# Performance work log

Measured on AMD Instinct MI355X. Metric: run time of the kernel, lower is better.

Reference implementation:

```python
import jax, jax.numpy as jnp
import numpy as np

EPS = 1e-5

def _make_mask(rng, outdim, indim, expand_size, k=3):
    # Mirrors ExpanderConv2d mask construction (indim <= outdim branch when equal)
    m = np.zeros((outdim, indim), dtype=np.float32)
    if indim > outdim:
        for i in range(outdim):
            idx = rng.permutation(indim)[:expand_size]
            m[i, idx] = 1.0
    else:
        for i in range(indim):
            idx = rng.permutation(outdim)[:expand_size]
            m[idx, i] = 1.0
    return jnp.asarray(np.broadcast_to(m[:, :, None, None], (outdim, indim, k, k)).copy())

def _bn(x, gamma, beta, mean, var):
    # eval-mode BatchNorm2d over channel axis (NCHW)
    inv = gamma / jnp.sqrt(var + EPS)
    return x * inv[None, :, None, None] + (beta - mean * inv)[None, :, None, None]

def _conv3x3(x, w, stride=1):
    return jax.lax.conv_general_dilated(
        x, w, window_strides=(stride, stride), padding=((1, 1), (1, 1)),
        dimension_numbers=('NCHW', 'OIHW', 'NCHW'))

def setup_inputs() -> dict:
    key = jax.random.key(0)
    ks = jax.random.split(key, 4)
    C = 256
    x = jax.random.normal(ks[0], (64, C, 32, 32), dtype=jnp.float32)
    fan_out = C * 9
    std = float(np.sqrt(2.0 / fan_out))  # kaiming_normal_, mode='fan_out'
    w1 = jax.random.normal(ks[1], (C, C, 3, 3), dtype=jnp.float32) * std
    w2 = jax.random.normal(ks[2], (C, C, 3, 3), dtype=jnp.float32) * std
    rng = np.random.default_rng(0)
    mask1 = _make_mask(rng, C, C, C // 8)
    mask2 = _make_mask(rng, C, C, C // 8)
    g = jax.random.uniform(ks[3], (4 * C,), minval=0.5, maxval=1.5, dtype=jnp.float32)
    return {
        'x': x,
        'bn1_gamma': g[:C], 'bn1_beta': jnp.zeros((C,), jnp.float32),
        'bn1_mean': jnp.zeros((C,), jnp.float32), 'bn1_var': jnp.ones((C,), jnp.float32),
        'w1': w1, 'mask1': mask1,
        'bn2_gamma': g[C:2 * C], 'bn2_beta': jnp.zeros((C,), jnp.float32),
        'bn2_mean': jnp.zeros((C,), jnp.float32), 'bn2_var': jnp.ones((C,), jnp.float32),
        'w2': w2, 'mask2': mask2,
    }

def reference(x, bn1_gamma, bn1_beta, bn1_mean, bn1_var, w1, mask1,
              bn2_gamma, bn2_beta, bn2_mean, bn2_var, w2, mask2):
    out = jax.nn.relu(_bn(x, bn1_gamma, bn1_beta, bn1_mean, bn1_var))
    out = _conv3x3(out, w1 * mask1)          # masked expander conv, dropout(p=0)=identity
    out = jax.nn.relu(_bn(out, bn2_gamma, bn2_beta, bn2_mean, bn2_var))
    out = _conv3x3(out, w2 * mask2, stride=1)
    return out + x                            # identity shortcut (stride=1, in==out)
```

## Files before the change

### kernel.cpp

```cpp
#include <hip/hip_runtime.h>
#include <hip/hip_bf16.h>
#include <stdint.h>

typedef __bf16 bf16_t;
typedef __bf16 bf16x8 __attribute__((ext_vector_type(8)));
typedef __bf16 bf16x4 __attribute__((ext_vector_type(4)));
typedef float  f32x4  __attribute__((ext_vector_type(4)));

#define AS_GLOBAL __attribute__((address_space(1)))
#define AS_LDS    __attribute__((address_space(3)))
#define VMW(N) asm volatile("s_waitcnt vmcnt(" #N ")" ::: "memory")

static constexpr int CCH   = 256;
static constexpr int HP    = 34;
static constexpr int PLANE = HP * HP;

__global__ void prep_params_k(const float* g1, const float* b1, const float* m1, const float* v1,
                              const float* g2, const float* b2, const float* m2, const float* v2,
                              float* prm) {
  int i = threadIdx.x;
  float i1 = g1[i] * rsqrtf(v1[i] + 1e-5f);
  prm[i]       = i1;
  prm[256 + i] = b1[i] - m1[i] * i1;
  float i2 = g2[i] * rsqrtf(v2[i] + 1e-5f);
  prm[512 + i] = i2;
  prm[768 + i] = b2[i] - m2[i] * i2;
}

__global__ __launch_bounds__(256) void prep_weights_k(const float* __restrict__ w,
                                                      const float* __restrict__ msk,
                                                      bf16_t* __restrict__ out) {
  int idx = blockIdx.x * 256 + threadIdx.x;
  const float* wp = w + (long)idx * 9;
  const float* mp = msk + (long)idx * 9;
#pragma unroll
  for (int khw = 0; khw < 9; ++khw)
    out[khw * 65536 + idx] = (bf16_t)(wp[khw] * mp[khw]);
}

__global__ __launch_bounds__(256) void zero_borders_k(bf16_t* __restrict__ t0p,
                                                      bf16_t* __restrict__ t1p) {
  const int bid = blockIdx.x;
  bf16_t* base = ((bid & 1) ? t1p : t0p) + (long)(bid >> 1) * PLANE * CCH;
  for (int i = threadIdx.x; i < 132 * 32; i += 256) {
    int pix = i >> 5, c16 = i & 31;
    int r, col;
    if (pix < 34)       { r = 0;           col = pix; }
    else if (pix < 68)  { r = 33;          col = pix - 34; }
    else if (pix < 100) { r = pix - 68 + 1; col = 0; }
    else                { r = pix - 100 + 1; col = 33; }
    *(f32x4*)&base[(r * HP + col) * CCH + c16 * 8] = f32x4{0.f, 0.f, 0.f, 0.f};
  }
}

__global__ __launch_bounds__(256) void prep_input_k(const float* __restrict__ x,
                                                    const float* __restrict__ prm,
                                                    bf16_t* __restrict__ t0p) {
  __shared__ __align__(16) bf16_t tile[64 * 256];
  const int tid = threadIdx.x;
  const int bid = blockIdx.x;
  const int n   = bid >> 4;
  const int p0  = (bid & 15) << 6;
  const int px    = tid & 63;
  const int cbase = tid >> 6;
  for (int r = 0; r < 64; ++r) {
    int ci = r * 4 + cbase;
    float v = x[((n * 256 + ci) << 10) + p0 + px];
    float y = fmaxf(v * prm[ci] + prm[256 + ci], 0.f);
    int byte = px * 512 + ((ci * 2) ^ ((px & 7) << 4));
    *(bf16_t*)((char*)tile + byte) = (bf16_t)y;
  }
  __syncthreads();
  for (int j = 0; j < 8; ++j) {
    int off  = j * 256 + tid;
    int pix  = off >> 5;
    int c16  = off & 31;
    int byte = pix * 512 + ((c16 * 16) ^ ((pix & 7) << 4));
    bf16x8 v = *(const bf16x8*)((char*)tile + byte);
    int p = p0 + pix;
    long gp = ((long)n * PLANE + ((p >> 5) + 1) * HP + (p & 31) + 1) * CCH + c16 * 8;
    *(bf16x8*)(t0p + gp) = v;
  }
}

template <int EPI>
__global__ __launch_bounds__(256, 2) void conv3x3_k(const bf16_t* __restrict__ inp,
                                                    const bf16_t* __restrict__ wts,
                                                    const float* __restrict__ prm,
                                                    const float* __restrict__ resid,
                                                    bf16_t* __restrict__ out_cl,
                                                    float* __restrict__ out_f) {
  __shared__ __align__(128) bf16_t As[5][4096];
  __shared__ __align__(128) bf16_t Bs[2][8192];

  const int tid  = threadIdx.x;
  const int lane = tid & 63;
  const int wid  = tid >> 6;
  const int wm   = wid >> 1;
  const int wn   = wid & 1;

  const int bid = blockIdx.x;
  const int w   = ((bid & 7) << 7) + (bid >> 3);
  const int co0 = (w & 1) << 7;
  const int pt  = w >> 1;
  const int n   = pt >> 3;
  const int hb  = (pt & 7) << 2;

  const int swz8 = (((lane & 3) ^ ((lane >> 2) & 3) ^ (lane >> 4)) << 3);
  const int l15  = lane & 15;
  const int k4   = lane >> 4;

  f32x4 acc[4][4];
#pragma unroll
  for (int i = 0; i < 4; ++i)
#pragma unroll
    for (int j = 0; j < 4; ++j) acc[i][j] = f32x4{0.f, 0.f, 0.f, 0.f};

  auto stageA = [&](int abuf, int c, int t) {
    const int ci0 = c << 5;
#pragma unroll
    for (int j = 0; j < 2; ++j) {
      const int ch  = wid * 2 + j;
      const int row = ch * 16 + (lane >> 2);
      const bf16_t* ga = wts + ((t * CCH + co0 + row) * CCH + ci0 + swz8);
      __builtin_amdgcn_global_load_lds((const AS_GLOBAL void*)ga,
                                       (AS_LDS void*)(&As[abuf][ch * 512]), 16, 0, 0);
    }
  };

  auto stageB = [&](int bbuf, int c) {
    const int ci0 = c << 5;
#pragma unroll
    for (int j = 0; j < 4; ++j) {
      const int ibase = wid * 4 + j;
      int s = (ibase << 6) + lane;
      if (s > 815) s = 815;
      const int r     = s / 136;
      const int rem   = s - r * 136;
      const int cc    = rem >> 2;
      const int k     = ((rem & 3) - (cc >> 1)) & 3;
      const bf16_t* gb = inp + ((n * PLANE + (hb + r) * HP + cc) * CCH + ci0 + (k << 3));
      __builtin_amdgcn_global_load_lds((const AS_GLOBAL void*)gb,
                                       (AS_LDS void*)(&Bs[bbuf][ibase * 512]), 16, 0, 0);
    }
  };

  auto compute = [&](int abuf, int bbuf, int kh, int kw) {
    bf16x8 av[4], bv[4];
#pragma unroll
    for (int mi = 0; mi < 4; ++mi)
      av[mi] = *(const bf16x8*)&As[abuf][((wm * 64 + mi * 16 + l15) << 5) + swz8];
#pragma unroll
    for (int ni = 0; ni < 4; ++ni) {
      const int p    = (wn << 6) + (ni << 4) + l15;
      const int cc   = (p & 31) + kw;
      const int slot = ((p >> 5) + kh) * 136 + (cc << 2) + ((k4 + (cc >> 1)) & 3);
      bv[ni] = *(const bf16x8*)&Bs[bbuf][slot << 3];
    }
#pragma unroll
    for (int mi = 0; mi < 4; ++mi)
#pragma unroll
      for (int ni = 0; ni < 4; ++ni)
        acc[mi][ni] = __builtin_amdgcn_mfma_f32_16x16x32_bf16(av[mi], bv[ni], acc[mi][ni], 0, 0, 0);
  };

  stageB(0, 0);
  stageA(0, 0, 0); stageA(1, 0, 1); stageA(2, 0, 2); stageA(3, 0, 3);

  int ab = 0;
  for (int c = 0; c < 7; ++c) {
#pragma unroll
    for (int t = 0; t < 9; ++t) {
      if (t >= 1 && t <= 3) { VMW(10); } else { VMW(6); }
      __builtin_amdgcn_s_barrier();
      if (t == 0) stageB((c + 1) & 1, c + 1);
      int aw = ab + 4; if (aw >= 5) aw -= 5;
      if (t < 5) stageA(aw, c, t + 4);
      else       stageA(aw, c + 1, t - 5);
      compute(ab, c & 1, t / 3, t % 3);
      ++ab; if (ab == 5) ab = 0;
    }
  }
#pragma unroll
  for (int t = 0; t < 9; ++t) {
    if      (t == 6) { VMW(4); }
    else if (t == 7) { VMW(2); }
    else if (t == 8) { VMW(0); }
    else             { VMW(6); }
    __builtin_amdgcn_s_barrier();
    if (t < 5) { int aw = ab + 4; if (aw >= 5) aw -= 5; stageA(aw, 7, t + 4); }
    compute(ab, 1, t / 3, t % 3);
    ++ab; if (ab == 5) ab = 0;
  }

  if (EPI == 0) {
#pragma unroll
    for (int mi = 0; mi < 4; ++mi) {
      const int co_b = co0 + wm * 64 + mi * 16 + ((lane >> 4) << 2);
      const float s0 = prm[co_b], s1 = prm[co_b + 1], s2 = prm[co_b + 2], s3 = prm[co_b + 3];
      const float t0 = prm[256 + co_b], t1 = prm[256 + co_b + 1],
                  t2 = prm[256 + co_b + 2], t3 = prm[256 + co_b + 3];
#pragma unroll
      for (int ni = 0; ni < 4; ++ni) {
        f32x4 v = acc[mi][ni];
        const int p  = (wn << 6) + (ni << 4) + l15;
        const int pr = p >> 5, pc = p & 31;
        bf16x4 pk;
        pk[0] = (bf16_t)fmaxf(v[0] * s0 + t0, 0.f);
        pk[1] = (bf16_t)fmaxf(v[1] * s1 + t1, 0.f);
        pk[2] = (bf16_t)fmaxf(v[2] * s2 + t2, 0.f);
        pk[3] = (bf16_t)fmaxf(v[3] * s3 + t3, 0.f);
        *(bf16x4*)&out_cl[(n * PLANE + (hb + pr + 1) * HP + pc + 1) * CCH + co_b] = pk;
      }
    }
  } else {
#pragma unroll
    for (int mi = 0; mi < 4; ++mi) {
      const int co_b = co0 + wm * 64 + mi * 16 + ((lane >> 4) << 2);
#pragma unroll
      for (int ni = 0; ni < 4; ++ni) {
        f32x4 v = acc[mi][ni];
        const int p  = (wn << 6) + (ni << 4) + l15;
        const int gp = ((n * CCH + co_b) << 10) + (hb << 5) + p;
        out_f[gp]        = v[0] + resid[gp];
        out_f[gp + 1024] = v[1] + resid[gp + 1024];
        out_f[gp + 2048] = v[2] + resid[gp + 2048];
        out_f[gp + 3072] = v[3] + resid[gp + 3072];
      }
    }
  }
}

extern "C" void kernel_launch(void* const* d_in, const int* in_sizes, int n_in,
                              void* d_out, int out_size, void* d_ws, size_t ws_size,
                              hipStream_t stream) {
  const float* x  = (const float*)d_in[0];
  const float* g1 = (const float*)d_in[1];
  const float* b1 = (const float*)d_in[2];
  const float* m1 = (const float*)d_in[3];
  const float* v1 = (const float*)d_in[4];
  const float* w1 = (const float*)d_in[5];
  const float* k1 = (const float*)d_in[6];
  const float* g2 = (const float*)d_in[7];
  const float* b2 = (const float*)d_in[8];
  const float* m2 = (const float*)d_in[9];
  const float* v2 = (const float*)d_in[10];
  const float* w2 = (const float*)d_in[11];
  const float* k2 = (const float*)d_in[12];

  char* ws = (char*)d_ws;
  const size_t T0P_B = (size_t)64 * PLANE * CCH * 2;
  bf16_t* t0p = (bf16_t*)ws;
  bf16_t* t1p = (bf16_t*)(ws + T0P_B);
  bf16_t* mw1 = (bf16_t*)(ws + 2 * T0P_B);
  bf16_t* mw2 = (bf16_t*)(ws + 2 * T0P_B + 1179648);
  float*  prm = (float*)(ws + 2 * T0P_B + 2 * 1179648);

  prep_params_k<<<1, 256, 0, stream>>>(g1, b1, m1, v1, g2, b2, m2, v2, prm);
  zero_borders_k<<<128, 256, 0, stream>>>(t0p, t1p);
  prep_weights_k<<<256, 256, 0, stream>>>(w1, k1, mw1);
  prep_weights_k<<<256, 256, 0, stream>>>(w2, k2, mw2);
  prep_input_k<<<1024, 256, 0, stream>>>(x, prm, t0p);

  conv3x3_k<0><<<1024, 256, 0, stream>>>(t0p, mw1, prm + 512, nullptr, t1p, nullptr);
  conv3x3_k<1><<<1024, 256, 0, stream>>>(t1p, mw2, nullptr, x, nullptr, (float*)d_out);
}
```

Before: 203.3 us.

## Double-buffer LDS fragment reads so next tap's loads overlap current MFMAs

Each tap's A/B fragments are now read from LDS into one of two register sets during the previous tap's iteration, and the MFMAs run on the other set. The whole K loop is fully unrolled with macros, and the vmcnt waits are retuned. The MFMA block is wrapped in setprio and a sched_barrier. The aim is to hide LDS read latency behind the matrix core work. The cost is higher register pressure and larger code, and the prefetch timing relative to the barriers has to stay correct for the buffer rotation.

```diff
diff --git a/kernel.cpp b/kernel.cpp
--- a/kernel.cpp
+++ b/kernel.cpp
@@ -116,6 +116,8 @@
 #pragma unroll
     for (int j = 0; j < 4; ++j) acc[i][j] = f32x4{0.f, 0.f, 0.f, 0.f};
 
+  bf16x8 avA[4], bvA[4], avB[4], bvB[4];
+
   auto stageA = [&](int abuf, int c, int t) {
     const int ci0 = c << 5;
 #pragma unroll
@@ -145,53 +147,74 @@
     }
   };
 
-  auto compute = [&](int abuf, int bbuf, int kh, int kw) {
-    bf16x8 av[4], bv[4];
-#pragma unroll
-    for (int mi = 0; mi < 4; ++mi)
-      av[mi] = *(const bf16x8*)&As[abuf][((wm * 64 + mi * 16 + l15) << 5) + swz8];
-#pragma unroll
-    for (int ni = 0; ni < 4; ++ni) {
-      const int p    = (wn << 6) + (ni << 4) + l15;
-      const int cc   = (p & 31) + kw;
-      const int slot = ((p >> 5) + kh) * 136 + (cc << 2) + ((k4 + (cc >> 1)) & 3);
-      bv[ni] = *(const bf16x8*)&Bs[bbuf][slot << 3];
-    }
-#pragma unroll
-    for (int mi = 0; mi < 4; ++mi)
-#pragma unroll
-      for (int ni = 0; ni < 4; ++ni)
-        acc[mi][ni] = __builtin_amdgcn_mfma_f32_16x16x32_bf16(av[mi], bv[ni], acc[mi][ni], 0, 0, 0);
-  };
+#define PREF(AV, BV, ABUF, BB, KH, KW) do {                                        \
+    _Pragma("unroll") for (int mi = 0; mi < 4; ++mi)                               \
+      AV[mi] = *(const bf16x8*)&As[ABUF][((wm * 64 + mi * 16 + l15) << 5) + swz8]; \
+    _Pragma("unroll") for (int ni = 0; ni < 4; ++ni) {                             \
+      const int p_    = (wn << 6) + (ni << 4) + l15;                               \
+      const int cc_   = (p_ & 31) + (KW);                                          \
+      const int slot_ = ((p_ >> 5) + (KH)) * 136 + (cc_ << 2) + ((k4 + (cc_ >> 1)) & 3); \
+      BV[ni] = *(const bf16x8*)&Bs[BB][slot_ << 3];                                \
+    }                                                                              \
+  } while (0)
+
+#define MFMA16(AV, BV) do {                                                        \
+    _Pragma("unroll") for (int mi = 0; mi < 4; ++mi)                               \
+    _Pragma("unroll") for (int ni = 0; ni < 4; ++ni)                               \
+      acc[mi][ni] = __builtin_amdgcn_mfma_f32_16x16x32_bf16(AV[mi], BV[ni], acc[mi][ni], 0, 0, 0); \
+  } while (0)
+
+#define PH(t, PAR, c, LAST) do {                                                   \
+    if ((LAST) && (t) >= 6) { if ((t) == 6) { VMW(2); } else { VMW(0); } }         \
+    else if (!(LAST) && ((t) == 1 || (t) == 2)) { VMW(8); }                        \
+    else { VMW(4); }                                                               \
+    __builtin_amdgcn_s_barrier();                                                  \
+    if (!(LAST) && (t) == 0) stageB(((c) + 1) & 1, (c) + 1);                       \
+    {                                                                              \
+      int aw = ab + 4; if (aw >= 5) aw -= 5;                                       \
+      if (!(LAST)) { if ((t) < 5) stageA(aw, (c), (t) + 4);                        \
+                     else         stageA(aw, (c) + 1, (t) - 5); }                  \
+      else if ((t) < 5) stageA(aw, 7, (t) + 4);                                    \
+    }                                                                              \
+    if (!((LAST) && (t) == 8)) {                                                   \
+      int ab1 = ab + 1; if (ab1 >= 5) ab1 -= 5;                                    \
+      const int bb1 = ((t) < 8 ? (c) & 1 : ((c) + 1) & 1);                         \
+      constexpr int T1 = ((t) + 1) % 9;                                            \
+      if (((PAR) + (t)) & 1) { PREF(avA, bvA, ab1, bb1, T1 / 3, T1 % 3); }         \
+      else                   { PREF(avB, bvB, ab1, bb1, T1 / 3, T1 % 3); }         \
+      asm volatile("s_waitcnt lgkmcnt(8)" ::: "memory");                           \
+    } else {                                                                       \
+      asm volatile("s_waitcnt lgkmcnt(0)" ::: "memory");                           \
+    }                                                                              \
+    __builtin_amdgcn_sched_barrier(0);                                             \
+    __builtin_amdgcn_s_setprio(1);                                                 \
+    if (((PAR) + (t)) & 1) { MFMA16(avB, bvB); } else { MFMA16(avA, bvA); }        \
+    __builtin_amdgcn_s_setprio(0);                                                 \
+    ++ab; if (ab == 5) ab = 0;                                                     \
+  } while (0)
+
+#define CHUNK(PAR, c) do {                                                         \
+    PH(0, PAR, c, 0); PH(1, PAR, c, 0); PH(2, PAR, c, 0);                          \
+    PH(3, PAR, c, 0); PH(4, PAR, c, 0); PH(5, PAR, c, 0);                          \
+    PH(6, PAR, c, 0); PH(7, PAR, c, 0); PH(8, PAR, c, 0);                          \
+  } while (0)
 
   stageB(0, 0);
   stageA(0, 0, 0); stageA(1, 0, 1); stageA(2, 0, 2); stageA(3, 0, 3);
+  VMW(6);
+  __builtin_amdgcn_s_barrier();
+  PREF(avA, bvA, 0, 0, 0, 0);
 
   int ab = 0;
-  for (int c = 0; c < 7; ++c) {
-#pragma unroll
-    for (int t = 0; t < 9; ++t) {
-      if (t >= 1 && t <= 3) { VMW(10); } else { VMW(6); }
-      __builtin_amdgcn_s_barrier();
-      if (t == 0) stageB((c + 1) & 1, c + 1);
-      int aw = ab + 4; if (aw >= 5) aw -= 5;
-      if (t < 5) stageA(aw, c, t + 4);
-      else       stageA(aw, c + 1, t - 5);
-      compute(ab, c & 1, t / 3, t % 3);
-      ++ab; if (ab == 5) ab = 0;
-    }
-  }
-#pragma unroll
-  for (int t = 0; t < 9; ++t) {
-    if      (t == 6) { VMW(4); }
-    else if (t == 7) { VMW(2); }
-    else if (t == 8) { VMW(0); }
-    else             { VMW(6); }
-    __builtin_amdgcn_s_barrier();
-    if (t < 5) { int aw = ab + 4; if (aw >= 5) aw -= 5; stageA(aw, 7, t + 4); }
-    compute(ab, 1, t / 3, t % 3);
-    ++ab; if (ab == 5) ab = 0;
-  }
+  CHUNK(0, 0); CHUNK(1, 1); CHUNK(0, 2); CHUNK(1, 3);
+  CHUNK(0, 4); CHUNK(1, 5); CHUNK(0, 6);
+  PH(0, 1, 7, 1); PH(1, 1, 7, 1); PH(2, 1, 7, 1); PH(3, 1, 7, 1); PH(4, 1, 7, 1);
+  PH(5, 1, 7, 1); PH(6, 1, 7, 1); PH(7, 1, 7, 1); PH(8, 1, 7, 1);
+
+#undef PH
+#undef CHUNK
+#undef PREF
+#undef MFMA16
 
   if (EPI == 0) {
 #pragma unroll
```

Measured after the change: 192.9 us. 1.05x faster.

## Shrink A-tile pipeline to double buffer, raise occupancy to 3 blocks, add setprio

Applied to the files above, without the earlier changes.

Cuts the weight (A) staging ring from five LDS buffers to two and raises launch bounds to allow three blocks per CU. The aim is to hide latency through extra waves instead of deep per-block prefetching. Waits are tightened to vmcnt(0)/vmcnt(4), so each block overlaps loads with compute less. MFMA sections are wrapped in s_setprio to favour the compute waves, and the outer chunk loop is no longer unrolled to save code size and registers.

```diff
diff --git a/kernel.cpp b/kernel.cpp
--- a/kernel.cpp
+++ b/kernel.cpp
@@ -84,13 +84,13 @@
 }
 
 template <int EPI>
-__global__ __launch_bounds__(256, 2) void conv3x3_k(const bf16_t* __restrict__ inp,
+__global__ __launch_bounds__(256, 3) void conv3x3_k(const bf16_t* __restrict__ inp,
                                                     const bf16_t* __restrict__ wts,
                                                     const float* __restrict__ prm,
                                                     const float* __restrict__ resid,
                                                     bf16_t* __restrict__ out_cl,
                                                     float* __restrict__ out_f) {
-  __shared__ __align__(128) bf16_t As[5][4096];
+  __shared__ __align__(128) bf16_t As[2][4096];
   __shared__ __align__(128) bf16_t Bs[2][8192];
 
   const int tid  = threadIdx.x;
@@ -145,53 +145,52 @@
     }
   };
 
-  auto compute = [&](int abuf, int bbuf, int kh, int kw) {
+  auto compute = [&](int ab, int bb, int kh, int kw) {
     bf16x8 av[4], bv[4];
 #pragma unroll
     for (int mi = 0; mi < 4; ++mi)
-      av[mi] = *(const bf16x8*)&As[abuf][((wm * 64 + mi * 16 + l15) << 5) + swz8];
+      av[mi] = *(const bf16x8*)&As[ab][((wm * 64 + mi * 16 + l15) << 5) + swz8];
 #pragma unroll
     for (int ni = 0; ni < 4; ++ni) {
       const int p    = (wn << 6) + (ni << 4) + l15;
       const int cc   = (p & 31) + kw;
       const int slot = ((p >> 5) + kh) * 136 + (cc << 2) + ((k4 + (cc >> 1)) & 3);
-      bv[ni] = *(const bf16x8*)&Bs[bbuf][slot << 3];
-    }
+      bv[ni] = *(const bf16x8*)&Bs[bb][slot << 3];
+    }
+    __builtin_amdgcn_s_setprio(1);
 #pragma unroll
     for (int mi = 0; mi < 4; ++mi)
 #pragma unroll
       for (int ni = 0; ni < 4; ++ni)
         acc[mi][ni] = __builtin_amdgcn_mfma_f32_16x16x32_bf16(av[mi], bv[ni], acc[mi][ni], 0, 0, 0);
+    __builtin_amdgcn_s_setprio(0);
   };
 
+#define PH(t, LASTC) do {                                                          \
+    if ((t) == 1 && !(LASTC)) { VMW(4); } else { VMW(0); }                         \
+    __builtin_amdgcn_s_barrier();                                                  \
+    {                                                                              \
+      const int pn = c * 9 + (t) + 1;                                              \
+      if (pn < 72) stageA(pn & 1, pn / 9, pn % 9);                                 \
+      if ((t) == 0 && !(LASTC)) stageB((c + 1) & 1, c + 1);                        \
+    }                                                                              \
+    compute((c * 9 + (t)) & 1, c & 1, (t) / 3, (t) % 3);                           \
+  } while (0)
+
   stageB(0, 0);
-  stageA(0, 0, 0); stageA(1, 0, 1); stageA(2, 0, 2); stageA(3, 0, 3);
-
-  int ab = 0;
+  stageA(0, 0, 0);
+
+#pragma unroll 1
   for (int c = 0; c < 7; ++c) {
-#pragma unroll
-    for (int t = 0; t < 9; ++t) {
-      if (t >= 1 && t <= 3) { VMW(10); } else { VMW(6); }
-      __builtin_amdgcn_s_barrier();
-      if (t == 0) stageB((c + 1) & 1, c + 1);
-      int aw = ab + 4; if (aw >= 5) aw -= 5;
-      if (t < 5) stageA(aw, c, t + 4);
-      else       stageA(aw, c + 1, t - 5);
-      compute(ab, c & 1, t / 3, t % 3);
-      ++ab; if (ab == 5) ab = 0;
-    }
-  }
-#pragma unroll
-  for (int t = 0; t < 9; ++t) {
-    if      (t == 6) { VMW(4); }
-    else if (t == 7) { VMW(2); }
-    else if (t == 8) { VMW(0); }
-    else             { VMW(6); }
-    __builtin_amdgcn_s_barrier();
-    if (t < 5) { int aw = ab + 4; if (aw >= 5) aw -= 5; stageA(aw, 7, t + 4); }
-    compute(ab, 1, t / 3, t % 3);
-    ++ab; if (ab == 5) ab = 0;
-  }
+    PH(0, 0); PH(1, 0); PH(2, 0); PH(3, 0); PH(4, 0);
+    PH(5, 0); PH(6, 0); PH(7, 0); PH(8, 0);
+  }
+  {
+    const int c = 7;
+    PH(0, 1); PH(1, 1); PH(2, 1); PH(3, 1); PH(4, 1);
+    PH(5, 1); PH(6, 1); PH(7, 1); PH(8, 1);
+  }
+#undef PH
 
   if (EPI == 0) {
 #pragma unroll
```

Measured after the change: 225.5 us. 10.9% more time.
